# Kernel tuning notes

Hardware: AMD Instinct MI355X
Metric: run time of the kernel (lower is better)

The kernel has to match this reference:

```python
import jax, jax.numpy as jnp
import numpy as np
import math

B, T, V, A, D = 8, 128, 32000, 64, 256
NS, S, H = 16, 128, 4
HD = D // H
SCALE = math.sqrt(HD)


def _ln(x, g, b):
    m = x.mean(-1, keepdims=True)
    xc = x - m
    v = (xc * xc).mean(-1, keepdims=True)
    return xc * jax.lax.rsqrt(v + 1e-5) * g + b


def setup_inputs() -> dict:
    key = jax.random.key(0)
    ks = iter(jax.random.split(key, 64))
    def w(shape, s=0.02):
        return jax.random.normal(next(ks), shape, jnp.float32) * s
    return dict(
        idx=jax.random.randint(next(ks), (B, T), 0, V),
        emb=w((V, D)), pos=w((S, D)),
        Wsens=w((D, NS * D)), bsens=jnp.zeros((NS * D,), jnp.float32),
        Wfb=w((V, D)), bfb=jnp.zeros((D,), jnp.float32),
        Wfg=w((2 * D, D)), bfg=jnp.zeros((D,), jnp.float32),
        bind=w((NS, D)),
        anet=w((2, A, A)),
        Wg=w((2, 2 * D, D)), bg=jnp.zeros((2, D), jnp.float32),
        Wc=w((2, D, D)), bc=jnp.zeros((2, D), jnp.float32),
        lng=jnp.ones((2, D), jnp.float32), lnb=jnp.zeros((2, D), jnp.float32),
        cmix=jnp.ones((2,), jnp.float32) / 2, aimp=w((A,)),
        Wq=w((D, D)), bq=jnp.zeros((D,), jnp.float32),
        Wk=w((D, D)), bk=jnp.zeros((D,), jnp.float32),
        Wv=w((D, D)), bv=jnp.zeros((D,), jnp.float32),
        Wo=w((D, D)), bo=jnp.zeros((D,), jnp.float32),
        Wmg=w((2 * D, D)), bmg=jnp.zeros((D,), jnp.float32),
        mlng=jnp.ones((D,), jnp.float32), mlnb=jnp.zeros((D,), jnp.float32),
        Wa1=w((D, 2 * D)), ba1=jnp.zeros((2 * D,), jnp.float32),
        Wa2=w((2 * D, V)), ba2=jnp.zeros((V,), jnp.float32),
    )


def _forward(idx, emb, pos, Wsens, bsens, Wfb, bfb, Wfg, bfg, bind, anet,
             Wg, bg, Wc, bc, lng, lnb, cmix, aimp, Wq, bq, Wk, bk, Wv, bv,
             Wo, bo, Wmg, bmg, mlng, mlnb, Wa1, ba1, Wa2, ba2):
    percepts = emb[idx] + pos[:T][None]            # [B,T,D]
    iw = jax.nn.softmax(aimp)                      # [A]
    cw = jax.nn.softmax(cmix)                      # [2]
    sig_bind = jax.nn.sigmoid(bind)                # [NS,D]
    slot_ids = jnp.arange(S)

    def step(carry, pt):
        agents, prev_logits, mem, t = carry
        # feedback gating of percept
        fb = prev_logits @ Wfb + bfb
        fg = jax.nn.sigmoid(jnp.concatenate([fb, pt], -1) @ Wfg + bfg)
        mod = pt * (1 + fg)
        sens = (mod @ Wsens + bsens).reshape(B, NS, D) * sig_bind
        agents = agents.at[:, :NS].add(sens)
        # two swarm channels, mixed
        new = 0.
        for c in range(2):
            inter = jnp.einsum('ij,bjd->bid', anet[c], agents)
            cand = jax.nn.gelu(inter @ Wc[c] + bc[c], approximate=False)
            gate = jax.nn.sigmoid(jnp.concatenate([agents, inter], -1) @ Wg[c] + bg[c])
            new = new + cw[c] * _ln(gate * cand + (1 - gate) * agents, lng[c], lnb[c])
        agents = new
        cons = jnp.einsum('bad,a->bd', agents, iw)  # [B,D]
        # holographic memory attention over valid slots (< t)
        Q = (cons @ Wq + bq).reshape(B, 1, H, HD)
        K = (mem @ Wk + bk).reshape(B, S, H, HD)
        Vv = (mem @ Wv + bv).reshape(B, S, H, HD)
        scores = jnp.einsum('bqhd,bshd->bhqs', Q, K) / SCALE  # [B,H,1,S]
        valid = slot_ids < t
        scores = jnp.where(valid[None, None, None, :], scores, -1e9)
        attn = jax.nn.softmax(scores, -1)
        rec = jnp.einsum('bhqs,bshd->bqhd', attn, Vv).reshape(B, D)
        rec = rec @ Wo + bo
        mgate = jax.nn.sigmoid(jnp.concatenate([cons, rec], -1) @ Wmg + bmg)
        attended = _ln(cons + mgate * rec, mlng, mlnb)
        cons = jnp.where(t > 0, attended, cons)
        # write detached consensus to slot t (T == MEMORY_SLOTS)
        mem = jax.lax.dynamic_update_slice(
            mem, jax.lax.stop_gradient(cons)[:, None, :], (0, t, 0))
        h = jax.nn.gelu(cons @ Wa1 + ba1, approximate=False)
        logits = h @ Wa2 + ba2
        return (agents, jax.lax.stop_gradient(logits), mem, t + 1), logits

    carry0 = (jnp.zeros((B, A, D), jnp.float32),
              jnp.zeros((B, V), jnp.float32),
              jnp.zeros((B, S, D), jnp.float32),
              jnp.int32(0))
    _, logits = jax.lax.scan(step, carry0, percepts.transpose(1, 0, 2))
    return logits.transpose(1, 0, 2)  # [B,T,V]


def reference(idx, emb, pos, Wsens, bsens, Wfb, bfb, Wfg, bfg, bind, anet,
              Wg, bg, Wc, bc, lng, lnb, cmix, aimp, Wq, bq, Wk, bk, Wv, bv,
              Wo, bo, Wmg, bmg, mlng, mlnb, Wa1, ba1, Wa2, ba2):
    return _forward(idx, emb, pos, Wsens, bsens, Wfb, bfb, Wfg, bfg, bind,
                    anet, Wg, bg, Wc, bc, lng, lnb, cmix, aimp, Wq, bq, Wk,
                    bk, Wv, bv, Wo, bo, Wmg, bmg, mlng, mlnb, Wa1, ba1,
                    Wa2, ba2)
```

## Files before the change

kernel.cpp:

```cpp
#include <hip/hip_runtime.h>
#include <math.h>

#define DEV __device__ __forceinline__

constexpr int B = 8, T = 128, V = 32000, A = 64, D = 256, NS = 16, S = 128, H = 4, HD = 64;
constexpr int D2 = 512;

DEV float sigm(float x) { return 1.0f / (1.0f + expf(-x)); }
DEV float geluf(float x) { return 0.5f * x * (1.0f + erff(x * 0.7071067811865476f)); }

DEV float4 f4z() { return make_float4(0.f, 0.f, 0.f, 0.f); }
DEV float4 ld4(const float* s) { return *(const float4*)s; }
DEV void st4(float* d, float4 v) { *(float4*)d = v; }
DEV float4 fma4(float a, float4 b, float4 c) {
  c.x += a * b.x; c.y += a * b.y; c.z += a * b.z; c.w += a * b.w; return c;
}
DEV float4 add4(float4 a, float4 b) {
  a.x += b.x; a.y += b.y; a.z += b.z; a.w += b.w; return a;
}
DEV float4 shflx4(float4 v, int m) {
  v.x = __shfl_xor(v.x, m, 64); v.y = __shfl_xor(v.y, m, 64);
  v.z = __shfl_xor(v.z, m, 64); v.w = __shfl_xor(v.w, m, 64); return v;
}

DEV void ast8(float* p, float x, float y) {
  union { float f[2]; unsigned long long u; } v;
  v.f[0] = x; v.f[1] = y;
  __hip_atomic_store((unsigned long long*)p, v.u, __ATOMIC_RELAXED, __HIP_MEMORY_SCOPE_AGENT);
}
DEV float2 ald8(const float* p) {
  unsigned long long u =
      __hip_atomic_load((const unsigned long long*)p, __ATOMIC_RELAXED, __HIP_MEMORY_SCOPE_AGENT);
  union { unsigned long long u; float f[2]; } v;
  v.u = u;
  return make_float2(v.f[0], v.f[1]);
}


__global__ __launch_bounds__(256) void k_setup(const float* __restrict__ aimp,
                                               const float* __restrict__ cmix,
                                               const float* __restrict__ bind,
                                               const float* __restrict__ bsens,
                                               float* __restrict__ iw, float* __restrict__ cwv,
                                               float* __restrict__ sigbind,
                                               float* __restrict__ bs2) {
  int tid = threadIdx.x;
  if (tid < 64) {
    float v = aimp[tid];
    float m = v;
    #pragma unroll
    for (int o = 32; o > 0; o >>= 1) m = fmaxf(m, __shfl_xor(m, o, 64));
    float e = expf(v - m);
    float s = e;
    #pragma unroll
    for (int o = 32; o > 0; o >>= 1) s += __shfl_xor(s, o, 64);
    iw[tid] = e / s;
  }
  if (tid == 0) {
    float a = cmix[0], b = cmix[1], m = fmaxf(a, b);
    float ea = expf(a - m), eb = expf(b - m);
    cwv[0] = ea / (ea + eb);
    cwv[1] = eb / (ea + eb);
  }
  for (int i = tid; i < NS * D; i += 256) {
    float sb = sigm(bind[i]);
    sigbind[i] = sb;
    bs2[i] = bsens[i] * sb;
  }
}

__global__ __launch_bounds__(256) void k_percepts(const int* __restrict__ idx,
                                                  const float* __restrict__ emb,
                                                  const float* __restrict__ pos,
                                                  float* __restrict__ P) {
  int i = blockIdx.x * 256 + threadIdx.x;
  if (i < B * T * D) {
    int d = i & (D - 1);
    int bt = i / D;
    int t = bt & (T - 1);
    P[i] = emb[(size_t)idx[bt] * D + d] + pos[t * D + d];
  }
}

__global__ __launch_bounds__(256) void k_cvec_part(const float* __restrict__ Wfb,
                                                   const float* __restrict__ ba2,
                                                   float* __restrict__ part) {
  int p = blockIdx.x, tid = threadIdx.x;
  int v0 = p * 256;
  float acc = 0.f;
  for (int vv = 0; vv < 256; vv++) acc += ba2[v0 + vv] * Wfb[(size_t)(v0 + vv) * D + tid];
  part[p * 256 + tid] = acc;
}

__global__ __launch_bounds__(256) void k_cvec_red(const float* __restrict__ part,
                                                  const float* __restrict__ bfb,
                                                  float* __restrict__ cvec) {
  int tid = threadIdx.x;
  float s = 0.f;
  for (int p = 0; p < 125; p++) s += part[p * 256 + tid];
  cvec[tid] = s + bfb[tid];
}

__global__ __launch_bounds__(256) void k_mpart(const float* __restrict__ Wa2,
                                               const float* __restrict__ Wfb,
                                               float* __restrict__ part) {
  int it = blockIdx.y;
  int vc = blockIdx.x;
  int j = threadIdx.x;
  int i0 = it * 32, v0 = vc * 4000;
  __shared__ float a_l[32 * 125];
  float acc[32];
  #pragma unroll
  for (int r = 0; r < 32; r++) acc[r] = 0.f;
  for (int vb = 0; vb < 4000; vb += 125) {
    for (int l = threadIdx.x; l < 32 * 125; l += 256) {
      int r = l / 125, c = l - r * 125;
      a_l[l] = Wa2[(size_t)(i0 + r) * V + v0 + vb + c];
    }
    __syncthreads();
    for (int c = 0; c < 125; c++) {
      float w = Wfb[(size_t)(v0 + vb + c) * D + j];
      #pragma unroll
      for (int r = 0; r < 32; r++) acc[r] += a_l[r * 125 + c] * w;
    }
    __syncthreads();
  }
  for (int r = 0; r < 32; r++) part[((size_t)vc * D2 + i0 + r) * D + j] = acc[r];
}

__global__ __launch_bounds__(256) void k_mreduce(const float* __restrict__ part,
                                                 float* __restrict__ M) {
  int i = blockIdx.x, j = threadIdx.x;
  float s = 0.f;
  for (int vc = 0; vc < 8; vc++) s += part[((size_t)vc * D2 + i) * D + j];
  M[i * D + j] = s;
}

__global__ __launch_bounds__(256) void k_gemmK256(const float* __restrict__ Am,
                                                  const float* __restrict__ Bm,
                                                  float* __restrict__ C, int I) {
  int r0 = blockIdx.x * 8;
  int tid = threadIdx.x;
  __shared__ float a_l[8][256];
  for (int i = tid; i < 8 * 256; i += 256) a_l[i >> 8][i & 255] = Am[(r0 + (i >> 8)) * 256 + (i & 255)];
  __syncthreads();
  float acc[8] = {0, 0, 0, 0, 0, 0, 0, 0};
  for (int k = 0; k < 256; k++) {
    float bv = Bm[k * 256 + tid];
    #pragma unroll
    for (int r = 0; r < 8; r++) acc[r] += a_l[r][k] * bv;
  }
  for (int r = 0; r < 8; r++) C[(r0 + r) * 256 + tid] = acc[r];
}

__global__ __launch_bounds__(256) void k_vecmat(const float* __restrict__ a,
                                                const float* __restrict__ Bm,
                                                const float* __restrict__ bias,
                                                float* __restrict__ out) {
  int tid = threadIdx.x;
  __shared__ float a_l[256];
  a_l[tid] = a[tid];
  __syncthreads();
  float acc = 0.f;
  for (int k = 0; k < 256; k++) acc += a_l[k] * Bm[k * 256 + tid];
  out[tid] = acc + bias[tid];
}

__global__ __launch_bounds__(256) void k_barinit(unsigned* bars) {
  int i = blockIdx.x * 256 + threadIdx.x;
  if (i < 8192) bars[i] = 0u;
}


DEV void cbar(unsigned* f, int slot, unsigned e) {
  __syncthreads();
  if (threadIdx.x == 0) {
    asm volatile("s_waitcnt vmcnt(0) lgkmcnt(0)" ::: "memory");
    __hip_atomic_store(&f[slot * 32], e, __ATOMIC_RELAXED, __HIP_MEMORY_SCOPE_AGENT);
  }
  if (threadIdx.x < 64) {
    int s = threadIdx.x & 31;
    unsigned spins = 0;
    for (;;) {
      unsigned v = __hip_atomic_load(&f[s * 32], __ATOMIC_RELAXED, __HIP_MEMORY_SCOPE_AGENT);
      if (__all(v >= e)) break;
      __builtin_amdgcn_s_sleep(1);
      if (++spins > (1u << 25)) break;
    }
  }
  __syncthreads();
}


struct PP {
  const float *Wsens, *bs2, *sigbind, *anet, *Wc, *bc, *Wg, *bg, *lng, *lnb, *cw, *iw;
  const float *Wq, *bq, *Wk, *bk, *Wv, *bv, *Wo, *bo, *Wmg, *WoMg, *cvec2, *mlng, *mlnb;
  const float *Wa1, *ba1, *M2, *cvec3, *cvec4, *P, *pW;
  float *agents, *sensbuf, *ubufG, *psumU, *consbuf, *recbuf, *valbuf, *valps;
  float *kvK, *kvV, *hbuf, *modbuf, *Hall;
  unsigned* flags;
};

#define A_OFF 0
#define ASL_OFF 8224
#define X_OFF 9248
#define U_OFF 12320
#define MOD_OFF 13344
#define CONS_OFF 13600
#define REC_OFF 13856
#define VV_OFF 14112
#define CF_OFF 14368
#define HL_OFF 14624
#define STT_OFF 15136
#define RED_OFF 15392
#define K_OFF 16416
#define V_OFF 24736
#define TOTAL_LDS_F 32928

__global__ __launch_bounds__(512) void k_persist(PP p) {
  extern __shared__ float sm[];
  const int bid = blockIdx.x;
  const int tid = threadIdx.x;
  const int b = bid & 7;
  const int slot = bid >> 3;
  const int ch = slot >> 4;
  const int i16 = slot & 15;
  const int d0 = i16 * 16;
  unsigned* flg = p.flags + b * 1024;
  unsigned e = 1;

  float* A_l = sm + A_OFF;
  float* Asl = sm + ASL_OFF;
  float* X_l = sm + X_OFF;
  float* U_l = sm + U_OFF;
  float* MODL = sm + MOD_OFF;
  float* CONSL = sm + CONS_OFF;
  float* RECL = sm + REC_OFF;
  float* VVL = sm + VV_OFF;
  float* CFL = sm + CF_OFF;
  float* HLL = sm + HL_OFF;
  float* STT = sm + STT_OFF;
  float* RED = sm + RED_OFF;
  float* K_l = sm + K_OFF;
  float* V_l = sm + V_OFF;

  if (tid < 256) ast8(p.agents + b * 16384 + slot * 512 + tid * 2, 0.f, 0.f);
  if (tid < 4) {
    int c = slot * 8 + tid * 2;
    int o = (b * 128) * 256 + c;
    float m0 = p.P[o] * (1.f + sigm(p.cvec4[c] + p.pW[o]));
    float m1 = p.P[o + 1] * (1.f + sigm(p.cvec4[c + 1] + p.pW[o + 1]));
    ast8(p.modbuf + b * 256 + c, m0, m1);
  }
  cbar(flg, slot, e); e++;

  for (int t = 0; t < T; t++) {
    {
      if (tid < 128) {
        float2 v = ald8(p.modbuf + b * 256 + tid * 2);
        MODL[tid * 2] = v.x; MODL[tid * 2 + 1] = v.y;
      }
      if (slot < 4 && t >= 1) {
        if (tid >= 128 && tid < 160) {
          int i2 = (tid - 128) * 2;
          float2 v = ald8(p.kvK + b * 256 + slot * 64 + i2);
          K_l[(t - 1) * 65 + i2] = v.x; K_l[(t - 1) * 65 + i2 + 1] = v.y;
        } else if (tid >= 160 && tid < 192) {
          int i2 = (tid - 160) * 2;
          float2 v = ald8(p.kvV + b * 256 + slot * 64 + i2);
          V_l[(t - 1) * 64 + i2] = v.x; V_l[(t - 1) * 64 + i2 + 1] = v.y;
        }
      }
      __syncthreads();
      {
        int cc = tid & 127, ks = tid >> 7;
        int col = slot * 128 + cc;
        float acc = 0.f;
        #pragma unroll 16
        for (int kk = 0; kk < 64; kk++) {
          int k = ks + kk * 4;
          acc += MODL[k] * p.Wsens[k * 4096 + col];
        }
        RED[ks * 128 + cc] = acc;
      }
      __syncthreads();
      if (tid < 64) {
        int c2 = tid * 2;
        int col = slot * 128 + c2;
        float s0 = RED[c2] + RED[128 + c2] + RED[256 + c2] + RED[384 + c2];
        float s1 = RED[c2 + 1] + RED[128 + c2 + 1] + RED[256 + c2 + 1] + RED[384 + c2 + 1];
        ast8(p.sensbuf + b * 4096 + col,
             s0 * p.sigbind[col] + p.bs2[col],
             s1 * p.sigbind[col + 1] + p.bs2[col + 1]);
      }
    }
    cbar(flg, slot, e); e++;

    {
      for (int half = 0; half < 2; half++) {
        for (int u = tid; u < 4096; u += 512) {
          int gu = half * 4096 + u;
          float2 v = ald8(p.agents + b * 16384 + gu * 2);
          if (half == 0 && u < 2048) {
            float2 s = ald8(p.sensbuf + b * 4096 + u * 2);
            v.x += s.x; v.y += s.y;
          }
          int r = u >> 7, kp = (u & 127) * 2;
          A_l[r * 257 + kp] = v.x; A_l[r * 257 + kp + 1] = v.y;
        }
        __syncthreads();
        {
          int r = tid >> 4, dc = tid & 15;
          Asl[(half * 32 + r) * 16 + dc] = A_l[r * 257 + d0 + dc];
        }
        {
          int r = tid >> 4, dq = (tid >> 2) & 3, ks = tid & 3;
          float4 ac = f4z(), ag0 = f4z(), ag1 = f4z();
          const float* wc = p.Wc + ch * 65536 + d0 + dq * 4;
          const float* wg0 = p.Wg + ch * 131072 + d0 + dq * 4;
          const float* wg1 = wg0 + 65536;
          #pragma unroll 8
          for (int kk = 0; kk < 64; kk++) {
            int k = ks + kk * 4;
            float a = A_l[r * 257 + k];
            ac = fma4(a, ld4(wc + k * 256), ac);
            ag0 = fma4(a, ld4(wg0 + k * 256), ag0);
            ag1 = fma4(a, ld4(wg1 + k * 256), ag1);
          }
          ac = add4(ac, shflx4(ac, 1)); ag0 = add4(ag0, shflx4(ag0, 1)); ag1 = add4(ag1, shflx4(ag1, 1));
          ac = add4(ac, shflx4(ac, 2)); ag0 = add4(ag0, shflx4(ag0, 2)); ag1 = add4(ag1, shflx4(ag1, 2));
          if (ks == 0) {
            int rr = half * 32 + r;
            st4(&X_l[rr * 48 + dq * 4], ac);
            st4(&X_l[rr * 48 + 16 + dq * 4], ag0);
            st4(&X_l[rr * 48 + 32 + dq * 4], ag1);
          }
        }
        __syncthreads();
      }
      {
        int r = tid >> 3, dq = (tid >> 1) & 3, js = tid & 1;
        float4 yc = f4z(), yg = f4z();
        const float* an = p.anet + ch * 4096 + r * 64;
        #pragma unroll 8
        for (int jj = 0; jj < 32; jj++) {
          int j = js + jj * 2;
          float a = an[j];
          yc = fma4(a, ld4(&X_l[j * 48 + dq * 4]), yc);
          yg = fma4(a, ld4(&X_l[j * 48 + 32 + dq * 4]), yg);
        }
        yc = add4(yc, shflx4(yc, 1));
        yg = add4(yg, shflx4(yg, 1));
        float su = 0.f, sq = 0.f;
        if (js == 0) {
          int c0g = d0 + dq * 4;
          float4 xg0 = ld4(&X_l[r * 48 + 16 + dq * 4]);
          float4 av = ld4(&Asl[r * 16 + dq * 4]);
          float4 bc4 = ld4(p.bc + ch * 256 + c0g);
          float4 bg4 = ld4(p.bg + ch * 256 + c0g);
          float4 uu;
          {
            float g0 = sigm(xg0.x + yg.x + bg4.x), c0c = geluf(yc.x + bc4.x);
            uu.x = g0 * c0c + (1.f - g0) * av.x;
            float g1 = sigm(xg0.y + yg.y + bg4.y), c1c = geluf(yc.y + bc4.y);
            uu.y = g1 * c1c + (1.f - g1) * av.y;
            float g2 = sigm(xg0.z + yg.z + bg4.z), c2c = geluf(yc.z + bc4.z);
            uu.z = g2 * c2c + (1.f - g2) * av.z;
            float g3 = sigm(xg0.w + yg.w + bg4.w), c3c = geluf(yc.w + bc4.w);
            uu.w = g3 * c3c + (1.f - g3) * av.w;
          }
          st4(&U_l[r * 16 + dq * 4], uu);
          su = uu.x + uu.y + uu.z + uu.w;
          sq = uu.x * uu.x + uu.y * uu.y + uu.z * uu.z + uu.w * uu.w;
        }
        su += __shfl_xor(su, 2, 64); sq += __shfl_xor(sq, 2, 64);
        su += __shfl_xor(su, 4, 64); sq += __shfl_xor(sq, 4, 64);
        if ((tid & 7) == 0)
          ast8(p.psumU + (((b * 2 + ch) * 16 + i16) * 64 + r) * 2, su, sq);
      }
      __syncthreads();
      if (ch == 1) {
        int r = tid >> 3, pp2 = tid & 7;
        ast8(p.ubufG + (((b * 16 + i16) * 64 + r) * 16) + pp2 * 2,
             U_l[r * 16 + pp2 * 2], U_l[r * 16 + pp2 * 2 + 1]);
      }
    }
    cbar(flg, slot, e); e++;

    if (ch == 0) {
      {
        int r = tid >> 3, pp2 = tid & 7;
        float2 v = ald8(p.ubufG + (((b * 16 + i16) * 64 + r) * 16) + pp2 * 2);
        X_l[r * 16 + pp2 * 2] = v.x; X_l[r * 16 + pp2 * 2 + 1] = v.y;
      }
      if (tid < 128) {
        int ch2 = tid >> 6, r = tid & 63;
        float s = 0.f, q = 0.f;
        #pragma unroll
        for (int blk = 0; blk < 16; blk++) {
          float2 v = ald8(p.psumU + (((b * 2 + ch2) * 16 + blk) * 64 + r) * 2);
          s += v.x; q += v.y;
        }
        float mn = s * (1.f / 256.f), var = q * (1.f / 256.f) - mn * mn;
        STT[(ch2 * 64 + r) * 2] = mn;
        STT[(ch2 * 64 + r) * 2 + 1] = rsqrtf(var + 1e-5f);
      }
      __syncthreads();
      {
        float cw0 = p.cw[0], cw1 = p.cw[1];
        int r = tid >> 3, pp2 = tid & 7;
        int c0g = d0 + pp2 * 2;
        float m0 = STT[r * 2], rs0 = STT[r * 2 + 1];
        float m1 = STT[128 + r * 2], rs1 = STT[128 + r * 2 + 1];
        float u0a = U_l[r * 16 + pp2 * 2], u0b = U_l[r * 16 + pp2 * 2 + 1];
        float u1a = X_l[r * 16 + pp2 * 2], u1b = X_l[r * 16 + pp2 * 2 + 1];
        float na = cw0 * ((u0a - m0) * rs0 * p.lng[c0g] + p.lnb[c0g]) +
                   cw1 * ((u1a - m1) * rs1 * p.lng[256 + c0g] + p.lnb[256 + c0g]);
        float nb = cw0 * ((u0b - m0) * rs0 * p.lng[c0g + 1] + p.lnb[c0g + 1]) +
                   cw1 * ((u1b - m1) * rs1 * p.lng[256 + c0g + 1] + p.lnb[256 + c0g + 1]);
        ast8(p.agents + (b * 64 + r) * 256 + c0g, na, nb);
        float iwr = p.iw[r];
        float pa = iwr * na, pb = iwr * nb;
        pa += __shfl_xor(pa, 8, 64); pb += __shfl_xor(pb, 8, 64);
        pa += __shfl_xor(pa, 16, 64); pb += __shfl_xor(pb, 16, 64);
        pa += __shfl_xor(pa, 32, 64); pb += __shfl_xor(pb, 32, 64);
        if ((tid & 63) < 8) {
          RED[(tid >> 6) * 8 + (tid & 7)] = pa;
          RED[64 + (tid >> 6) * 8 + (tid & 7)] = pb;
        }
      }
      __syncthreads();
      if (tid < 8) {
        float sa = 0.f, sb = 0.f;
        #pragma unroll
        for (int w = 0; w < 8; w++) { sa += RED[w * 8 + tid]; sb += RED[64 + w * 8 + tid]; }
        ast8(p.consbuf + b * 256 + d0 + tid * 2, sa, sb);
      }
    }
    cbar(flg, slot, e); e++;

    if (slot < 4 && t > 0) {
      int h = slot;
      if (tid < 128) {
        float2 v = ald8(p.consbuf + b * 256 + tid * 2);
        CONSL[tid * 2] = v.x; CONSL[tid * 2 + 1] = v.y;
      }
      __syncthreads();
      {
        int c = tid & 63, ks = tid >> 6;
        float acc = 0.f;
        #pragma unroll 8
        for (int kk = 0; kk < 32; kk++) {
          int k = ks + kk * 8;
          acc += CONSL[k] * p.Wq[k * 256 + h * 64 + c];
        }
        RED[ks * 64 + c] = acc;
      }
      __syncthreads();
      if (tid < 64) {
        float qv = p.bq[h * 64 + tid];
        #pragma unroll
        for (int w = 0; w < 8; w++) qv += RED[w * 64 + tid];
        VVL[tid] = qv;
      }
      __syncthreads();
      {
        int s = tid >> 2, ds = tid & 3;
        float acc = 0.f;
        if (s < t) {
          #pragma unroll
          for (int i2 = 0; i2 < 16; i2++) {
            int d = ds * 16 + i2;
            acc += VVL[d] * K_l[s * 65 + d];
          }
        }
        acc += __shfl_xor(acc, 1, 64);
        acc += __shfl_xor(acc, 2, 64);
        if (s < t && ds == 0) RECL[s] = acc * 0.125f;
      }
      __syncthreads();
      if (tid < 128) {
        float v = (tid < t) ? RECL[tid] : -1e30f;
        float m = v;
        #pragma unroll
        for (int o = 1; o < 64; o <<= 1) m = fmaxf(m, __shfl_xor(m, o, 64));
        if ((tid & 63) == 0) STT[tid >> 6] = m;
      }
      __syncthreads();
      if (tid < 128) {
        float m = fmaxf(STT[0], STT[1]);
        float v = (tid < t) ? RECL[tid] : -1e30f;
        float ee = (tid < t) ? expf(v - m) : 0.f;
        float den = ee;
        #pragma unroll
        for (int o = 1; o < 64; o <<= 1) den += __shfl_xor(den, o, 64);
        if ((tid & 63) == 0) STT[2 + (tid >> 6)] = den;
        CFL[tid] = ee;
      }
      __syncthreads();
      if (tid < 128) RECL[tid] = CFL[tid] / (STT[2] + STT[3]);
      __syncthreads();
      {
        int c = tid & 63, ss = tid >> 6;
        float acc = 0.f;
        #pragma unroll
        for (int i2 = 0; i2 < 16; i2++) {
          int s = ss + i2 * 8;
          if (s < t) acc += RECL[s] * V_l[s * 64 + c];
        }
        RED[ss * 64 + c] = acc;
      }
      __syncthreads();
      if (tid < 64) {
        float rv = 0.f;
        #pragma unroll
        for (int w = 0; w < 8; w++) rv += RED[w * 64 + tid];
        CFL[tid] = rv;
      }
      __syncthreads();
      if (tid < 32) ast8(p.recbuf + b * 256 + h * 64 + tid * 2, CFL[tid * 2], CFL[tid * 2 + 1]);
    }
    cbar(flg, slot, e); e++;

    if (slot >= 8 && slot < 16 && t > 0) {
      int j = slot - 8;
      if (tid < 128) {
        float2 v = ald8(p.recbuf + b * 256 + tid * 2);
        RECL[tid * 2] = v.x; RECL[tid * 2 + 1] = v.y;
        float2 w = ald8(p.consbuf + b * 256 + tid * 2);
        CONSL[tid * 2] = w.x; CONSL[tid * 2 + 1] = w.y;
      }
      __syncthreads();
      {
        int c = tid & 31, ks = tid >> 5;
        float po = 0.f, pm = 0.f;
        #pragma unroll
        for (int kk = 0; kk < 16; kk++) {
          int k = ks + kk * 16;
          float rv = RECL[k], cv = CONSL[k];
          po += rv * p.Wo[k * 256 + j * 32 + c];
          pm += cv * p.Wmg[k * 256 + j * 32 + c] + rv * p.WoMg[k * 256 + j * 32 + c];
        }
        RED[ks * 32 + c] = po;
        RED[512 + ks * 32 + c] = pm;
      }
      __syncthreads();
      if (tid < 32) {
        int col = j * 32 + tid;
        float so = p.bo[col], sm2 = p.cvec2[col];
        #pragma unroll
        for (int k2 = 0; k2 < 16; k2++) { so += RED[k2 * 32 + tid]; sm2 += RED[512 + k2 * 32 + tid]; }
        float mg = sigm(sm2);
        float val = CONSL[col] + mg * so;
        VVL[tid] = val;
        float su = val, sq = val * val;
        #pragma unroll
        for (int o2 = 1; o2 <= 16; o2 <<= 1) { su += __shfl_xor(su, o2, 64); sq += __shfl_xor(sq, o2, 64); }
        if (tid == 0) ast8(p.valps + (b * 8 + j) * 2, su, sq);
      }
      __syncthreads();
      if (tid < 16) ast8(p.valbuf + b * 256 + j * 32 + tid * 2, VVL[tid * 2], VVL[tid * 2 + 1]);
    }
    cbar(flg, slot, e); e++;

    if (slot >= 16 && slot < 24) {
      int jj = slot - 16;
      const float* src = (t > 0) ? p.valbuf : p.consbuf;
      if (tid < 128) {
        float2 v = ald8(src + b * 256 + tid * 2);
        VVL[tid * 2] = v.x; VVL[tid * 2 + 1] = v.y;
      }
      if (t > 0 && tid >= 128 && tid < 136) {
        float2 v = ald8(p.valps + (b * 8 + (tid - 128)) * 2);
        RED[(tid - 128) * 2] = v.x; RED[(tid - 128) * 2 + 1] = v.y;
      }
      __syncthreads();
      if (t > 0) {
        if (tid == 0) {
          float s = 0.f, q = 0.f;
          #pragma unroll
          for (int k2 = 0; k2 < 8; k2++) { s += RED[k2 * 2]; q += RED[k2 * 2 + 1]; }
          float mn = s * (1.f / 256.f), var = q * (1.f / 256.f) - mn * mn;
          STT[0] = mn; STT[1] = rsqrtf(var + 1e-5f);
        }
        __syncthreads();
        if (tid < 256) CFL[tid] = (VVL[tid] - STT[0]) * STT[1] * p.mlng[tid] + p.mlnb[tid];
      } else {
        if (tid < 256) CFL[tid] = VVL[tid];
      }
      __syncthreads();
      {
        int c = tid & 31, ks = tid >> 5;
        float pk = 0.f, pv = 0.f;
        #pragma unroll
        for (int kk = 0; kk < 16; kk++) {
          int k = ks + kk * 16;
          float cf = CFL[k];
          pk += cf * p.Wk[k * 256 + jj * 32 + c];
          pv += cf * p.Wv[k * 256 + jj * 32 + c];
        }
        RED[ks * 32 + c] = pk;
        RED[512 + ks * 32 + c] = pv;
      }
      __syncthreads();
      if (tid < 32) {
        int col = jj * 32 + tid;
        float sk = p.bk[col], sv = p.bv[col];
        #pragma unroll
        for (int k2 = 0; k2 < 16; k2++) { sk += RED[k2 * 32 + tid]; sv += RED[512 + k2 * 32 + tid]; }
        VVL[tid] = sk;
        VVL[64 + tid] = sv;
      }
      __syncthreads();
      if (tid < 16) {
        ast8(p.kvK + b * 256 + jj * 32 + tid * 2, VVL[tid * 2], VVL[tid * 2 + 1]);
        ast8(p.kvV + b * 256 + jj * 32 + tid * 2, VVL[64 + tid * 2], VVL[64 + tid * 2 + 1]);
      }
      __syncthreads();
      {
        int c = tid & 63, ks = tid >> 6;
        float ph = 0.f;
        #pragma unroll 8
        for (int kk = 0; kk < 32; kk++) {
          int k = ks + kk * 8;
          ph += CFL[k] * p.Wa1[k * 512 + jj * 64 + c];
        }
        RED[ks * 64 + c] = ph;
      }
      __syncthreads();
      if (tid < 64) {
        int col = jj * 64 + tid;
        float s = p.ba1[col];
        #pragma unroll
        for (int w = 0; w < 8; w++) s += RED[w * 64 + tid];
        float hv = geluf(s);
        HLL[tid] = hv;
        p.Hall[(size_t)(b * 128 + t) * 512 + col] = hv;
      }
      __syncthreads();
      if (tid < 32) ast8(p.hbuf + b * 512 + jj * 64 + tid * 2, HLL[tid * 2], HLL[tid * 2 + 1]);
    }
    cbar(flg, slot, e); e++;

    if (slot >= 24 && t < T - 1) {
      int jm = slot - 24;
      if (tid < 256) {
        float2 v = ald8(p.hbuf + b * 512 + tid * 2);
        HLL[tid * 2] = v.x; HLL[tid * 2 + 1] = v.y;
      }
      __syncthreads();
      {
        int c = tid & 31, ks = tid >> 5;
        float pf = 0.f;
        #pragma unroll 8
        for (int kk = 0; kk < 32; kk++) {
          int k = ks + kk * 16;
          pf += HLL[k] * p.M2[k * 256 + jm * 32 + c];
        }
        RED[ks * 32 + c] = pf;
      }
      __syncthreads();
      if (tid < 32) {
        int col = jm * 32 + tid;
        float s = p.cvec3[col];
        #pragma unroll
        for (int k2 = 0; k2 < 16; k2++) s += RED[k2 * 32 + tid];
        int o = (b * 128 + t + 1) * 256 + col;
        VVL[tid] = p.P[o] * (1.f + sigm(s + p.pW[o]));
      }
      __syncthreads();
      if (tid < 16) ast8(p.modbuf + b * 256 + jm * 32 + tid * 2, VVL[tid * 2], VVL[tid * 2 + 1]);
    }
    cbar(flg, slot, e); e++;
  }
}


__global__ __launch_bounds__(256) void k_logits(const float* __restrict__ Hall,
                                                const float* __restrict__ Wa2,
                                                const float* __restrict__ ba2,
                                                float* __restrict__ out) {
  int rt = blockIdx.y;
  int v = blockIdx.x * 256 + threadIdx.x;
  const float* hrow = Hall + (size_t)rt * 32 * D2;
  float acc[32];
  float bb = ba2[v];
  #pragma unroll
  for (int r = 0; r < 32; r++) acc[r] = bb;
  for (int k = 0; k < D2; k++) {
    float w = Wa2[(size_t)k * V + v];
    #pragma unroll
    for (int r = 0; r < 32; r++) acc[r] += hrow[r * D2 + k] * w;
  }
  for (int r = 0; r < 32; r++) out[(size_t)(rt * 32 + r) * V + v] = acc[r];
}


extern "C" void kernel_launch(void* const* d_in, const int* in_sizes, int n_in,
                              void* d_out, int out_size, void* d_ws, size_t ws_size,
                              hipStream_t stream) {
  const int* idx = (const int*)d_in[0];
  const float* emb = (const float*)d_in[1];
  const float* pos = (const float*)d_in[2];
  const float* Wsens = (const float*)d_in[3];
  const float* bsens = (const float*)d_in[4];
  const float* Wfb = (const float*)d_in[5];
  const float* bfb = (const float*)d_in[6];
  const float* Wfg = (const float*)d_in[7];
  const float* bfg = (const float*)d_in[8];
  const float* bind = (const float*)d_in[9];
  const float* anet = (const float*)d_in[10];
  const float* Wg = (const float*)d_in[11];
  const float* bg = (const float*)d_in[12];
  const float* Wc = (const float*)d_in[13];
  const float* bc = (const float*)d_in[14];
  const float* lng = (const float*)d_in[15];
  const float* lnb = (const float*)d_in[16];
  const float* cmix = (const float*)d_in[17];
  const float* aimp = (const float*)d_in[18];
  const float* Wq = (const float*)d_in[19];
  const float* bq = (const float*)d_in[20];
  const float* Wk = (const float*)d_in[21];
  const float* bk = (const float*)d_in[22];
  const float* Wv = (const float*)d_in[23];
  const float* bv = (const float*)d_in[24];
  const float* Wo = (const float*)d_in[25];
  const float* bo = (const float*)d_in[26];
  const float* Wmg = (const float*)d_in[27];
  const float* bmg = (const float*)d_in[28];
  const float* mlng = (const float*)d_in[29];
  const float* mlnb = (const float*)d_in[30];
  const float* Wa1 = (const float*)d_in[31];
  const float* ba1 = (const float*)d_in[32];
  const float* Wa2 = (const float*)d_in[33];
  const float* ba2 = (const float*)d_in[34];

  float* ws = (float*)d_ws;
  float* M2 = ws + 0;
  float* WoMg = ws + 131072;
  float* cvec = ws + 196608;
  float* cvec2 = ws + 196864;
  float* cvec3 = ws + 197120;
  float* cvec4 = ws + 197376;
  float* iw = ws + 197632;
  float* cwb = ws + 197696;
  float* sigbind = ws + 197760;
  float* bs2 = ws + 201856;
  float* P = ws + 205952;
  float* pW = ws + 468096;
  float* agents = ws + 730240;
  float* sensbuf = ws + 861312;
  float* ubufG = ws + 894080;
  float* psumU = ws + 1025152;
  float* consbuf = ws + 1057920;
  float* recbuf = ws + 1059968;
  float* valbuf = ws + 1062016;
  float* valps = ws + 1064064;
  float* kvK = ws + 1064192;
  float* kvV = ws + 1066240;
  float* hbuf = ws + 1068288;
  float* modbuf = ws + 1072384;
  float* Hall = ws + 1074432;
  float* M = ws + 1598720;
  float* Mpart = ws + 1729792;
  float* cvpart = ws + 2778368;
  unsigned* flags = (unsigned*)(ws + 2810368);

  k_setup<<<1, 256, 0, stream>>>(aimp, cmix, bind, bsens, iw, cwb, sigbind, bs2);
  k_percepts<<<dim3((B * T * D + 255) / 256), 256, 0, stream>>>(idx, emb, pos, P);
  k_cvec_part<<<125, 256, 0, stream>>>(Wfb, ba2, cvpart);
  k_cvec_red<<<1, 256, 0, stream>>>(cvpart, bfb, cvec);
  k_mpart<<<dim3(8, 16), 256, 0, stream>>>(Wa2, Wfb, Mpart);
  k_mreduce<<<512, 256, 0, stream>>>(Mpart, M);
  k_gemmK256<<<64, 256, 0, stream>>>(M, Wfg, M2, 512);
  k_gemmK256<<<32, 256, 0, stream>>>(Wo, Wmg + 65536, WoMg, 256);
  k_gemmK256<<<128, 256, 0, stream>>>(P, Wfg + 65536, pW, 1024);
  k_vecmat<<<1, 256, 0, stream>>>(bo, Wmg + 65536, bmg, cvec2);
  k_vecmat<<<1, 256, 0, stream>>>(cvec, Wfg, bfg, cvec3);
  k_vecmat<<<1, 256, 0, stream>>>(bfb, Wfg, bfg, cvec4);
  k_barinit<<<32, 256, 0, stream>>>(flags);

  PP prm;
  prm.Wsens = Wsens; prm.bs2 = bs2; prm.sigbind = sigbind; prm.anet = anet;
  prm.Wc = Wc; prm.bc = bc; prm.Wg = Wg; prm.bg = bg; prm.lng = lng; prm.lnb = lnb;
  prm.cw = cwb; prm.iw = iw; prm.Wq = Wq; prm.bq = bq; prm.Wk = Wk; prm.bk = bk;
  prm.Wv = Wv; prm.bv = bv; prm.Wo = Wo; prm.bo = bo; prm.Wmg = Wmg; prm.WoMg = WoMg;
  prm.cvec2 = cvec2; prm.mlng = mlng; prm.mlnb = mlnb; prm.Wa1 = Wa1; prm.ba1 = ba1;
  prm.M2 = M2; prm.cvec3 = cvec3; prm.cvec4 = cvec4; prm.P = P; prm.pW = pW;
  prm.agents = agents; prm.sensbuf = sensbuf; prm.ubufG = ubufG; prm.psumU = psumU;
  prm.consbuf = consbuf; prm.recbuf = recbuf; prm.valbuf = valbuf; prm.valps = valps;
  prm.kvK = kvK; prm.kvV = kvV; prm.hbuf = hbuf; prm.modbuf = modbuf;
  prm.Hall = Hall; prm.flags = flags;

  hipFuncSetAttribute((const void*)k_persist, hipFuncAttributeMaxDynamicSharedMemorySize,
                      TOTAL_LDS_F * 4);

  void* args[] = {&prm};
  hipLaunchCooperativeKernel((void*)k_persist, dim3(256), dim3(512), args,
                             TOTAL_LDS_F * 4, stream);

  k_logits<<<dim3(125, 32), 256, 0, stream>>>(Hall, Wa2, ba2, (float*)d_out);
}
```

Baseline: 27.95 ms.

## Replace 8-byte atomic inter-block exchanges with cache-bypassing dwordx4 loads and stores

All cross-block exchange buffers in the persistent kernel now use 16-byte global loads and stores with sc0 sc1 coherence bits, issued as inline asm, in place of 8-byte relaxed atomics. Several buffers (psumU, ubufG) are relaid out so each block reads or writes contiguous vectors. LDS row strides change from 257/65 to 260/68 so rows can take float4 stores. The K/V cache fill moves into the attention phase. The aim is fewer, wider memory transactions on the serial per-timestep critical path between grid barriers. The cost is reliance on hand-written asm coherence semantics, and the new padding may cause LDS bank conflicts.

```diff
diff --git a/kernel.cpp b/kernel.cpp
--- a/kernel.cpp
+++ b/kernel.cpp
@@ -6,34 +6,50 @@
 constexpr int B = 8, T = 128, V = 32000, A = 64, D = 256, NS = 16, S = 128, H = 4, HD = 64;
 constexpr int D2 = 512;
 
+typedef float f32x4 __attribute__((ext_vector_type(4)));
+typedef float f32x2 __attribute__((ext_vector_type(2)));
+
 DEV float sigm(float x) { return 1.0f / (1.0f + expf(-x)); }
 DEV float geluf(float x) { return 0.5f * x * (1.0f + erff(x * 0.7071067811865476f)); }
 
-DEV float4 f4z() { return make_float4(0.f, 0.f, 0.f, 0.f); }
-DEV float4 ld4(const float* s) { return *(const float4*)s; }
-DEV void st4(float* d, float4 v) { *(float4*)d = v; }
-DEV float4 fma4(float a, float4 b, float4 c) {
-  c.x += a * b.x; c.y += a * b.y; c.z += a * b.z; c.w += a * b.w; return c;
-}
-DEV float4 add4(float4 a, float4 b) {
-  a.x += b.x; a.y += b.y; a.z += b.z; a.w += b.w; return a;
-}
-DEV float4 shflx4(float4 v, int m) {
+DEV f32x4 f4z() { return f32x4{0.f, 0.f, 0.f, 0.f}; }
+DEV f32x4 ld4(const float* s) { return *(const f32x4*)s; }
+DEV void st4(float* d, f32x4 v) { *(f32x4*)d = v; }
+DEV f32x4 fma4(float a, f32x4 b, f32x4 c) { return c + a * b; }
+DEV f32x4 add4(f32x4 a, f32x4 b) { return a + b; }
+DEV f32x4 shflx4(f32x4 v, int m) {
   v.x = __shfl_xor(v.x, m, 64); v.y = __shfl_xor(v.y, m, 64);
   v.z = __shfl_xor(v.z, m, 64); v.w = __shfl_xor(v.w, m, 64); return v;
 }
 
-DEV void ast8(float* p, float x, float y) {
-  union { float f[2]; unsigned long long u; } v;
-  v.f[0] = x; v.f[1] = y;
-  __hip_atomic_store((unsigned long long*)p, v.u, __ATOMIC_RELAXED, __HIP_MEMORY_SCOPE_AGENT);
-}
-DEV float2 ald8(const float* p) {
-  unsigned long long u =
-      __hip_atomic_load((const unsigned long long*)p, __ATOMIC_RELAXED, __HIP_MEMORY_SCOPE_AGENT);
-  union { unsigned long long u; float f[2]; } v;
-  v.u = u;
-  return make_float2(v.f[0], v.f[1]);
+DEV f32x4 cld4(const float* p) {
+  f32x4 r;
+  asm volatile("global_load_dwordx4 %0, %1, off sc0 sc1\n"
+               "s_waitcnt vmcnt(0)"
+               : "=&v"(r) : "v"(p) : "memory");
+  return r;
+}
+DEV void cld4x2(const float* p0, const float* p1, f32x4& a, f32x4& b) {
+  asm volatile("global_load_dwordx4 %0, %2, off sc0 sc1\n"
+               "global_load_dwordx4 %1, %3, off sc0 sc1\n"
+               "s_waitcnt vmcnt(0)"
+               : "=&v"(a), "=&v"(b) : "v"(p0), "v"(p1) : "memory");
+}
+DEV void cld4x4(const float* p0, const float* p1, const float* p2, const float* p3,
+                f32x4& a, f32x4& b, f32x4& c, f32x4& d) {
+  asm volatile("global_load_dwordx4 %0, %4, off sc0 sc1\n"
+               "global_load_dwordx4 %1, %5, off sc0 sc1\n"
+               "global_load_dwordx4 %2, %6, off sc0 sc1\n"
+               "global_load_dwordx4 %3, %7, off sc0 sc1\n"
+               "s_waitcnt vmcnt(0)"
+               : "=&v"(a), "=&v"(b), "=&v"(c), "=&v"(d)
+               : "v"(p0), "v"(p1), "v"(p2), "v"(p3) : "memory");
+}
+DEV void cst4(float* p, f32x4 v) {
+  asm volatile("global_store_dwordx4 %0, %1, off sc0 sc1" :: "v"(p), "v"(v) : "memory");
+}
+DEV void cst2(float* p, f32x2 v) {
+  asm volatile("global_store_dwordx2 %0, %1, off sc0 sc1" :: "v"(p), "v"(v) : "memory");
 }
 
 
@@ -173,11 +189,10 @@
 
 
 DEV void cbar(unsigned* f, int slot, unsigned e) {
+  asm volatile("s_waitcnt vmcnt(0) lgkmcnt(0)" ::: "memory");
   __syncthreads();
-  if (threadIdx.x == 0) {
-    asm volatile("s_waitcnt vmcnt(0) lgkmcnt(0)" ::: "memory");
+  if (threadIdx.x == 0)
     __hip_atomic_store(&f[slot * 32], e, __ATOMIC_RELAXED, __HIP_MEMORY_SCOPE_AGENT);
-  }
   if (threadIdx.x < 64) {
     int s = threadIdx.x & 31;
     unsigned spins = 0;
@@ -202,20 +217,20 @@
 };
 
 #define A_OFF 0
-#define ASL_OFF 8224
-#define X_OFF 9248
-#define U_OFF 12320
-#define MOD_OFF 13344
-#define CONS_OFF 13600
-#define REC_OFF 13856
-#define VV_OFF 14112
-#define CF_OFF 14368
-#define HL_OFF 14624
-#define STT_OFF 15136
-#define RED_OFF 15392
-#define K_OFF 16416
-#define V_OFF 24736
-#define TOTAL_LDS_F 32928
+#define ASL_OFF 8320
+#define X_OFF 9344
+#define U_OFF 12416
+#define MOD_OFF 13440
+#define CONS_OFF 13696
+#define REC_OFF 13952
+#define VV_OFF 14208
+#define CF_OFF 14464
+#define HL_OFF 14720
+#define STT_OFF 15232
+#define RED_OFF 15488
+#define K_OFF 16512
+#define V_OFF 25216
+#define TOTAL_LDS_F 33408
 
 __global__ __launch_bounds__(512) void k_persist(PP p) {
   extern __shared__ float sm[];
@@ -244,33 +259,19 @@
   float* K_l = sm + K_OFF;
   float* V_l = sm + V_OFF;
 
-  if (tid < 256) ast8(p.agents + b * 16384 + slot * 512 + tid * 2, 0.f, 0.f);
+  if (tid < 128) cst4(p.agents + b * 16384 + slot * 512 + tid * 4, f4z());
   if (tid < 4) {
     int c = slot * 8 + tid * 2;
     int o = (b * 128) * 256 + c;
     float m0 = p.P[o] * (1.f + sigm(p.cvec4[c] + p.pW[o]));
     float m1 = p.P[o + 1] * (1.f + sigm(p.cvec4[c + 1] + p.pW[o + 1]));
-    ast8(p.modbuf + b * 256 + c, m0, m1);
+    cst2(p.modbuf + b * 256 + c, f32x2{m0, m1});
   }
   cbar(flg, slot, e); e++;
 
   for (int t = 0; t < T; t++) {
     {
-      if (tid < 128) {
-        float2 v = ald8(p.modbuf + b * 256 + tid * 2);
-        MODL[tid * 2] = v.x; MODL[tid * 2 + 1] = v.y;
-      }
-      if (slot < 4 && t >= 1) {
-        if (tid >= 128 && tid < 160) {
-          int i2 = (tid - 128) * 2;
-          float2 v = ald8(p.kvK + b * 256 + slot * 64 + i2);
-          K_l[(t - 1) * 65 + i2] = v.x; K_l[(t - 1) * 65 + i2 + 1] = v.y;
-        } else if (tid >= 160 && tid < 192) {
-          int i2 = (tid - 160) * 2;
-          float2 v = ald8(p.kvV + b * 256 + slot * 64 + i2);
-          V_l[(t - 1) * 64 + i2] = v.x; V_l[(t - 1) * 64 + i2 + 1] = v.y;
-        }
-      }
+      if (tid < 64) st4(&MODL[tid * 4], cld4(p.modbuf + b * 256 + tid * 4));
       __syncthreads();
       {
         int cc = tid & 127, ks = tid >> 7;
@@ -284,45 +285,53 @@
         RED[ks * 128 + cc] = acc;
       }
       __syncthreads();
-      if (tid < 64) {
-        int c2 = tid * 2;
-        int col = slot * 128 + c2;
-        float s0 = RED[c2] + RED[128 + c2] + RED[256 + c2] + RED[384 + c2];
-        float s1 = RED[c2 + 1] + RED[128 + c2 + 1] + RED[256 + c2 + 1] + RED[384 + c2 + 1];
-        ast8(p.sensbuf + b * 4096 + col,
-             s0 * p.sigbind[col] + p.bs2[col],
-             s1 * p.sigbind[col + 1] + p.bs2[col + 1]);
+      if (tid < 32) {
+        f32x4 sv;
+        #pragma unroll
+        for (int j = 0; j < 4; j++) {
+          int c4 = tid * 4 + j, col = slot * 128 + c4;
+          float s = RED[c4] + RED[128 + c4] + RED[256 + c4] + RED[384 + c4];
+          sv[j] = s * p.sigbind[col] + p.bs2[col];
+        }
+        cst4(p.sensbuf + b * 4096 + slot * 128 + tid * 4, sv);
       }
     }
     cbar(flg, slot, e); e++;
 
     {
       for (int half = 0; half < 2; half++) {
-        for (int u = tid; u < 4096; u += 512) {
-          int gu = half * 4096 + u;
-          float2 v = ald8(p.agents + b * 16384 + gu * 2);
-          if (half == 0 && u < 2048) {
-            float2 s = ald8(p.sensbuf + b * 4096 + u * 2);
-            v.x += s.x; v.y += s.y;
-          }
-          int r = u >> 7, kp = (u & 127) * 2;
-          A_l[r * 257 + kp] = v.x; A_l[r * 257 + kp + 1] = v.y;
+        const float* abase = p.agents + b * 16384 + half * 8192;
+        f32x4 va, vb, vc2, vd;
+        cld4x4(abase + tid * 4, abase + 2048 + tid * 4, abase + 4096 + tid * 4,
+               abase + 6144 + tid * 4, va, vb, vc2, vd);
+        if (half == 0) {
+          f32x4 s0, s1;
+          cld4x2(p.sensbuf + b * 4096 + tid * 4, p.sensbuf + b * 4096 + 2048 + tid * 4, s0, s1);
+          va = add4(va, s0);
+          vb = add4(vb, s1);
+        }
+        {
+          int f0 = tid, f1 = tid + 512, f2 = tid + 1024, f3 = tid + 1536;
+          st4(&A_l[(f0 >> 6) * 260 + (f0 & 63) * 4], va);
+          st4(&A_l[(f1 >> 6) * 260 + (f1 & 63) * 4], vb);
+          st4(&A_l[(f2 >> 6) * 260 + (f2 & 63) * 4], vc2);
+          st4(&A_l[(f3 >> 6) * 260 + (f3 & 63) * 4], vd);
         }
         __syncthreads();
         {
           int r = tid >> 4, dc = tid & 15;
-          Asl[(half * 32 + r) * 16 + dc] = A_l[r * 257 + d0 + dc];
+          Asl[(half * 32 + r) * 16 + dc] = A_l[r * 260 + d0 + dc];
         }
         {
           int r = tid >> 4, dq = (tid >> 2) & 3, ks = tid & 3;
-          float4 ac = f4z(), ag0 = f4z(), ag1 = f4z();
+          f32x4 ac = f4z(), ag0 = f4z(), ag1 = f4z();
           const float* wc = p.Wc + ch * 65536 + d0 + dq * 4;
           const float* wg0 = p.Wg + ch * 131072 + d0 + dq * 4;
           const float* wg1 = wg0 + 65536;
           #pragma unroll 8
           for (int kk = 0; kk < 64; kk++) {
             int k = ks + kk * 4;
-            float a = A_l[r * 257 + k];
+            float a = A_l[r * 260 + k];
             ac = fma4(a, ld4(wc + k * 256), ac);
             ag0 = fma4(a, ld4(wg0 + k * 256), ag0);
             ag1 = fma4(a, ld4(wg1 + k * 256), ag1);
@@ -340,7 +349,7 @@
       }
       {
         int r = tid >> 3, dq = (tid >> 1) & 3, js = tid & 1;
-        float4 yc = f4z(), yg = f4z();
+        f32x4 yc = f4z(), yg = f4z();
         const float* an = p.anet + ch * 4096 + r * 64;
         #pragma unroll 8
         for (int jj = 0; jj < 32; jj++) {
@@ -354,20 +363,16 @@
         float su = 0.f, sq = 0.f;
         if (js == 0) {
           int c0g = d0 + dq * 4;
-          float4 xg0 = ld4(&X_l[r * 48 + 16 + dq * 4]);
-          float4 av = ld4(&Asl[r * 16 + dq * 4]);
-          float4 bc4 = ld4(p.bc + ch * 256 + c0g);
-          float4 bg4 = ld4(p.bg + ch * 256 + c0g);
-          float4 uu;
-          {
-            float g0 = sigm(xg0.x + yg.x + bg4.x), c0c = geluf(yc.x + bc4.x);
-            uu.x = g0 * c0c + (1.f - g0) * av.x;
-            float g1 = sigm(xg0.y + yg.y + bg4.y), c1c = geluf(yc.y + bc4.y);
-            uu.y = g1 * c1c + (1.f - g1) * av.y;
-            float g2 = sigm(xg0.z + yg.z + bg4.z), c2c = geluf(yc.z + bc4.z);
-            uu.z = g2 * c2c + (1.f - g2) * av.z;
-            float g3 = sigm(xg0.w + yg.w + bg4.w), c3c = geluf(yc.w + bc4.w);
-            uu.w = g3 * c3c + (1.f - g3) * av.w;
+          f32x4 xg0 = ld4(&X_l[r * 48 + 16 + dq * 4]);
+          f32x4 av = ld4(&Asl[r * 16 + dq * 4]);
+          f32x4 bc4 = ld4(p.bc + ch * 256 + c0g);
+          f32x4 bg4 = ld4(p.bg + ch * 256 + c0g);
+          f32x4 uu;
+          #pragma unroll
+          for (int q = 0; q < 4; q++) {
+            float g = sigm(xg0[q] + yg[q] + bg4[q]);
+            float cnd = geluf(yc[q] + bc4[q]);
+            uu[q] = g * cnd + (1.f - g) * av[q];
           }
           st4(&U_l[r * 16 + dq * 4], uu);
           su = uu.x + uu.y + uu.z + uu.w;
@@ -376,31 +381,26 @@
         su += __shfl_xor(su, 2, 64); sq += __shfl_xor(sq, 2, 64);
         su += __shfl_xor(su, 4, 64); sq += __shfl_xor(sq, 4, 64);
         if ((tid & 7) == 0)
-          ast8(p.psumU + (((b * 2 + ch) * 16 + i16) * 64 + r) * 2, su, sq);
-      }
-      __syncthreads();
-      if (ch == 1) {
-        int r = tid >> 3, pp2 = tid & 7;
-        ast8(p.ubufG + (((b * 16 + i16) * 64 + r) * 16) + pp2 * 2,
-             U_l[r * 16 + pp2 * 2], U_l[r * 16 + pp2 * 2 + 1]);
-      }
+          cst2(p.psumU + ((b * 2 + ch) * 64 + r) * 32 + i16 * 2, f32x2{su, sq});
+      }
+      __syncthreads();
+      if (ch == 1 && tid < 256)
+        cst4(p.ubufG + (b * 16 + i16) * 1024 + tid * 4, ld4(&U_l[tid * 4]));
     }
     cbar(flg, slot, e); e++;
 
     if (ch == 0) {
-      {
-        int r = tid >> 3, pp2 = tid & 7;
-        float2 v = ald8(p.ubufG + (((b * 16 + i16) * 64 + r) * 16) + pp2 * 2);
-        X_l[r * 16 + pp2 * 2] = v.x; X_l[r * 16 + pp2 * 2 + 1] = v.y;
-      }
+      if (tid < 256) st4(&X_l[tid * 4], cld4(p.ubufG + (b * 16 + i16) * 1024 + tid * 4));
       if (tid < 128) {
         int ch2 = tid >> 6, r = tid & 63;
-        float s = 0.f, q = 0.f;
-        #pragma unroll
-        for (int blk = 0; blk < 16; blk++) {
-          float2 v = ald8(p.psumU + (((b * 2 + ch2) * 16 + blk) * 64 + r) * 2);
-          s += v.x; q += v.y;
-        }
+        const float* ps = p.psumU + ((b * 2 + ch2) * 64 + r) * 32;
+        f32x4 q0, q1, q2, q3, q4, q5, q6, q7;
+        cld4x4(ps, ps + 4, ps + 8, ps + 12, q0, q1, q2, q3);
+        cld4x4(ps + 16, ps + 20, ps + 24, ps + 28, q4, q5, q6, q7);
+        float s = q0.x + q0.z + q1.x + q1.z + q2.x + q2.z + q3.x + q3.z +
+                  q4.x + q4.z + q5.x + q5.z + q6.x + q6.z + q7.x + q7.z;
+        float q = q0.y + q0.w + q1.y + q1.w + q2.y + q2.w + q3.y + q3.w +
+                  q4.y + q4.w + q5.y + q5.w + q6.y + q6.w + q7.y + q7.w;
         float mn = s * (1.f / 256.f), var = q * (1.f / 256.f) - mn * mn;
         STT[(ch2 * 64 + r) * 2] = mn;
         STT[(ch2 * 64 + r) * 2 + 1] = rsqrtf(var + 1e-5f);
@@ -418,7 +418,7 @@
                    cw1 * ((u1a - m1) * rs1 * p.lng[256 + c0g] + p.lnb[256 + c0g]);
         float nb = cw0 * ((u0b - m0) * rs0 * p.lng[c0g + 1] + p.lnb[c0g + 1]) +
                    cw1 * ((u1b - m1) * rs1 * p.lng[256 + c0g + 1] + p.lnb[256 + c0g + 1]);
-        ast8(p.agents + (b * 64 + r) * 256 + c0g, na, nb);
+        cst2(p.agents + (b * 64 + r) * 256 + c0g, f32x2{na, nb});
         float iwr = p.iw[r];
         float pa = iwr * na, pb = iwr * nb;
         pa += __shfl_xor(pa, 8, 64); pb += __shfl_xor(pb, 8, 64);
@@ -434,17 +434,19 @@
         float sa = 0.f, sb = 0.f;
         #pragma unroll
         for (int w = 0; w < 8; w++) { sa += RED[w * 8 + tid]; sb += RED[64 + w * 8 + tid]; }
-        ast8(p.consbuf + b * 256 + d0 + tid * 2, sa, sb);
+        cst2(p.consbuf + b * 256 + d0 + tid * 2, f32x2{sa, sb});
       }
     }
     cbar(flg, slot, e); e++;
 
     if (slot < 4 && t > 0) {
       int h = slot;
-      if (tid < 128) {
-        float2 v = ald8(p.consbuf + b * 256 + tid * 2);
-        CONSL[tid * 2] = v.x; CONSL[tid * 2 + 1] = v.y;
-      }
+      if (tid < 16) st4(&K_l[(t - 1) * 68 + tid * 4], cld4(p.kvK + b * 256 + h * 64 + tid * 4));
+      else if (tid < 32) {
+        int q2 = tid - 16;
+        st4(&V_l[(t - 1) * 64 + q2 * 4], cld4(p.kvV + b * 256 + h * 64 + q2 * 4));
+      }
+      if (tid < 64) st4(&CONSL[tid * 4], cld4(p.consbuf + b * 256 + tid * 4));
       __syncthreads();
       {
         int c = tid & 63, ks = tid >> 6;
@@ -471,7 +473,7 @@
           #pragma unroll
           for (int i2 = 0; i2 < 16; i2++) {
             int d = ds * 16 + i2;
-            acc += VVL[d] * K_l[s * 65 + d];
+            acc += VVL[d] * K_l[s * 68 + d];
           }
         }
         acc += __shfl_xor(acc, 1, 64);
@@ -518,17 +520,17 @@
         CFL[tid] = rv;
       }
       __syncthreads();
-      if (tid < 32) ast8(p.recbuf + b * 256 + h * 64 + tid * 2, CFL[tid * 2], CFL[tid * 2 + 1]);
+      if (tid < 16) cst4(p.recbuf + b * 256 + h * 64 + tid * 4, ld4(&CFL[tid * 4]));
     }
     cbar(flg, slot, e); e++;
 
     if (slot >= 8 && slot < 16 && t > 0) {
       int j = slot - 8;
-      if (tid < 128) {
-        float2 v = ald8(p.recbuf + b * 256 + tid * 2);
-        RECL[tid * 2] = v.x; RECL[tid * 2 + 1] = v.y;
-        float2 w = ald8(p.consbuf + b * 256 + tid * 2);
-        CONSL[tid * 2] = w.x; CONSL[tid * 2 + 1] = w.y;
+      if (tid < 64) {
+        f32x4 r4, c4;
+        cld4x2(p.recbuf + b * 256 + tid * 4, p.consbuf + b * 256 + tid * 4, r4, c4);
+        st4(&RECL[tid * 4], r4);
+        st4(&CONSL[tid * 4], c4);
       }
       __syncthreads();
       {
@@ -556,24 +558,19 @@
         float su = val, sq = val * val;
         #pragma unroll
         for (int o2 = 1; o2 <= 16; o2 <<= 1) { su += __shfl_xor(su, o2, 64); sq += __shfl_xor(sq, o2, 64); }
-        if (tid == 0) ast8(p.valps + (b * 8 + j) * 2, su, sq);
-      }
-      __syncthreads();
-      if (tid < 16) ast8(p.valbuf + b * 256 + j * 32 + tid * 2, VVL[tid * 2], VVL[tid * 2 + 1]);
+        if (tid == 0) cst2(p.valps + b * 16 + j * 2, f32x2{su, sq});
+      }
+      __syncthreads();
+      if (tid < 8) cst4(p.valbuf + b * 256 + j * 32 + tid * 4, ld4(&VVL[tid * 4]));
     }
     cbar(flg, slot, e); e++;
 
     if (slot >= 16 && slot < 24) {
       int jj = slot - 16;
       const float* src = (t > 0) ? p.valbuf : p.consbuf;
-      if (tid < 128) {
-        float2 v = ald8(src + b * 256 + tid * 2);
-        VVL[tid * 2] = v.x; VVL[tid * 2 + 1] = v.y;
-      }
-      if (t > 0 && tid >= 128 && tid < 136) {
-        float2 v = ald8(p.valps + (b * 8 + (tid - 128)) * 2);
-        RED[(tid - 128) * 2] = v.x; RED[(tid - 128) * 2 + 1] = v.y;
-      }
+      if (tid < 64) st4(&VVL[tid * 4], cld4(src + b * 256 + tid * 4));
+      if (t > 0 && tid >= 64 && tid < 68)
+        st4(&RED[(tid - 64) * 4], cld4(p.valps + b * 16 + (tid - 64) * 4));
       __syncthreads();
       if (t > 0) {
         if (tid == 0) {
@@ -612,10 +609,8 @@
         VVL[64 + tid] = sv;
       }
       __syncthreads();
-      if (tid < 16) {
-        ast8(p.kvK + b * 256 + jj * 32 + tid * 2, VVL[tid * 2], VVL[tid * 2 + 1]);
-        ast8(p.kvV + b * 256 + jj * 32 + tid * 2, VVL[64 + tid * 2], VVL[64 + tid * 2 + 1]);
-      }
+      if (tid < 8) cst4(p.kvK + b * 256 + jj * 32 + tid * 4, ld4(&VVL[tid * 4]));
+      else if (tid < 16) cst4(p.kvV + b * 256 + jj * 32 + (tid - 8) * 4, ld4(&VVL[64 + (tid - 8) * 4]));
       __syncthreads();
       {
         int c = tid & 63, ks = tid >> 6;
@@ -638,16 +633,13 @@
         p.Hall[(size_t)(b * 128 + t) * 512 + col] = hv;
       }
       __syncthreads();
-      if (tid < 32) ast8(p.hbuf + b * 512 + jj * 64 + tid * 2, HLL[tid * 2], HLL[tid * 2 + 1]);
+      if (tid < 16) cst4(p.hbuf + b * 512 + jj * 64 + tid * 4, ld4(&HLL[tid * 4]));
     }
     cbar(flg, slot, e); e++;
 
     if (slot >= 24 && t < T - 1) {
       int jm = slot - 24;
-      if (tid < 256) {
-        float2 v = ald8(p.hbuf + b * 512 + tid * 2);
-        HLL[tid * 2] = v.x; HLL[tid * 2 + 1] = v.y;
-      }
+      if (tid < 128) st4(&HLL[tid * 4], cld4(p.hbuf + b * 512 + tid * 4));
       __syncthreads();
       {
         int c = tid & 31, ks = tid >> 5;
@@ -669,7 +661,7 @@
         VVL[tid] = p.P[o] * (1.f + sigm(s + p.pW[o]));
       }
       __syncthreads();
-      if (tid < 16) ast8(p.modbuf + b * 256 + jm * 32 + tid * 2, VVL[tid * 2], VVL[tid * 2 + 1]);
+      if (tid < 8) cst4(p.modbuf + b * 256 + jm * 32 + tid * 4, ld4(&VVL[tid * 4]));
     }
     cbar(flg, slot, e); e++;
   }
```

Measured after the change: 26.69 ms. 4.5% less time.
